# Kernel tuning notes

Hardware: AMD Instinct MI355X
Metric: run time of the kernel (lower is better)

Reference implementation:

```python
import jax, jax.numpy as jnp
import numpy as np

B, L, H, N = 8, 8192, 128, 32  # batch, seq_len, d_model, d_state//2 (complex)


def setup_inputs() -> dict:
    key = jax.random.key(0)
    ks = jax.random.split(key, 13)
    x = jax.random.normal(ks[0], (B, L, 2), dtype=jnp.float32)
    enc_w = jax.random.normal(ks[1], (2, H), dtype=jnp.float32) * (1.0 / np.sqrt(2.0))
    enc_b = jax.random.normal(ks[2], (H,), dtype=jnp.float32) * 0.01
    # S4D init: dt log-uniform in [1e-3, 1e-1], A = -0.5 + i*pi*n (S4D-Lin)
    u01 = jax.random.uniform(ks[3], (H,), dtype=jnp.float32)
    log_dt = u01 * (np.log(0.1) - np.log(0.001)) + np.log(0.001)
    log_A_real = jnp.full((H, N), np.log(0.5), dtype=jnp.float32)
    A_imag = jnp.broadcast_to(np.pi * jnp.arange(N, dtype=jnp.float32), (H, N)).copy()
    C_re = jax.random.normal(ks[4], (H, N), dtype=jnp.float32) * (0.5 ** 0.5)
    C_im = jax.random.normal(ks[5], (H, N), dtype=jnp.float32) * (0.5 ** 0.5)
    D = jax.random.normal(ks[6], (H,), dtype=jnp.float32)
    out_w = jax.random.normal(ks[7], (2 * H, H), dtype=jnp.float32) * (1.0 / np.sqrt(H))
    out_b = jax.random.normal(ks[8], (2 * H,), dtype=jnp.float32) * 0.01
    dec_w = jax.random.normal(ks[9], (H, 1), dtype=jnp.float32) * (1.0 / np.sqrt(H))
    dec_b = jax.random.normal(ks[10], (1,), dtype=jnp.float32) * 0.01
    return {"x": x, "enc_w": enc_w, "enc_b": enc_b, "log_dt": log_dt,
            "log_A_real": log_A_real, "A_imag": A_imag, "C_re": C_re,
            "C_im": C_im, "D": D, "out_w": out_w, "out_b": out_b,
            "dec_w": dec_w, "dec_b": dec_b}


def reference(x, enc_w, enc_b, log_dt, log_A_real, A_imag, C_re, C_im, D,
              out_w, out_b, dec_w, dec_b):
    # Encoder (B,L,2) -> (B,L,H), then transpose to channels-first (B,H,L)
    u = jnp.einsum('blc,ch->blh', x, enc_w) + enc_b
    u = jnp.swapaxes(u, -1, -2)  # (B,H,L)
    Lx = u.shape[-1]

    # --- S4D kernel (zero-order-hold discretization, diagonal A) ---
    dt = jnp.exp(log_dt)                      # (H,)
    A = -jnp.exp(log_A_real) + 1j * A_imag    # (H,N) complex
    C = C_re + 1j * C_im                      # (H,N)
    dtA = dt[:, None] * A                     # (H,N)
    K_coef = C * (jnp.exp(dtA) - 1.0) / A     # (H,N)
    # Vandermonde: exp(dtA * l), l = 0..L-1  -> (H,N,L)
    vand = jnp.exp(dtA[:, :, None] * jnp.arange(Lx, dtype=jnp.float32))
    K = 2.0 * jnp.einsum('hn,hnl->hl', K_coef, vand).real  # (H,L)

    # --- causal convolution via FFT (length 2L avoids circular wrap) ---
    n = 2 * Lx
    y = jnp.fft.irfft(jnp.fft.rfft(u, n) * jnp.fft.rfft(K, n), n)[..., :Lx]
    y = y + D[:, None] * u                    # skip connection

    # GELU -> pointwise GLU output projection (Conv1d(H, 2H, 1) + GLU)
    y = jax.nn.gelu(y)
    z = jnp.einsum('bhl,gh->bgl', y, out_w) + out_b[None, :, None]  # (B,2H,L)
    a, g = jnp.split(z, 2, axis=1)
    y = a * jax.nn.sigmoid(g)                 # (B,H,L)

    # Mean-pool over sequence, decode to scalar: (B,1)
    pooled = jnp.mean(y, axis=-1)             # (B,H)
    return pooled @ dec_w + dec_b
```

## Files before the change

kernel.cpp:

```cpp
#include <hip/hip_runtime.h>
#include <math.h>

#define B_ 8
#define L_ 8192
#define H_ 128
#define N_ 32
#define C_ 128
#define T_ 64


typedef _Float16 half8 __attribute__((ext_vector_type(8)));
typedef __attribute__((ext_vector_type(4))) float f32x4;

__device__ __forceinline__ float gelu_tanh(float y) {
    float t = 0.7978845608028654f * fmaf(0.044715f, y * y * y, y);
    float e = __expf(2.f * t);
    float th = 1.f - __fdividef(2.f, e + 1.f);
    return 0.5f * y * (1.f + th);
}
__device__ __forceinline__ unsigned short f2h(float f) {
    _Float16 h = (_Float16)f;
    return *(unsigned short*)&h;
}
__device__ __forceinline__ float h2f(unsigned short u) {
    return (float)(*(const _Float16*)&u);
}

__global__ __launch_bounds__(256) void k_s4d(
    const float* __restrict__ x, const float* __restrict__ enc_w,
    const float* __restrict__ enc_b, const float* __restrict__ log_dt,
    const float* __restrict__ log_A_real, const float* __restrict__ A_imag,
    const float* __restrict__ C_re, const float* __restrict__ C_im,
    const float* __restrict__ Dp, const float* __restrict__ out_w,
    unsigned short* __restrict__ Wh, unsigned short* __restrict__ gy)
{
    const int bh = blockIdx.x;
    const int b = bh >> 7, h = bh & (H_ - 1);
    const int tid = threadIdx.x;
    const int lane = tid & 63, wq = tid >> 6;
    const int mrow = lane & 15, quad = lane >> 4;

    __shared__ unsigned short Ut[C_][72];
    __shared__ __align__(16) char scratch[18432];
    __shared__ float2 wTpow[7][N_];
    __shared__ float2 coefs[N_];
    __shared__ float2 ArAi[N_];
    __shared__ float  Kd[64];
    unsigned short* E16 = (unsigned short*)scratch;
    float2*         Sx  = (float2*)scratch;
    unsigned short* St  = (unsigned short*)scratch;

    const float dt = expf(log_dt[h]);

    if (tid < N_) {
        int n = tid;
        float Ar = -expf(log_A_real[h * N_ + n]);
        float Ai = A_imag[h * N_ + n];
        ArAi[n] = make_float2(Ar, Ai);
        float ar = dt * Ar, ai = dt * Ai;
        float er = expf(ar);
        float wr = er * cosf(ai), wi = er * sinf(ai);
        float inv = 1.f / (Ar * Ar + Ai * Ai);
        float numr = wr - 1.f, numi = wi;
        float qr = (numr * Ar + numi * Ai) * inv;
        float qi = (numi * Ar - numr * Ai) * inv;
        coefs[n] = make_float2(C_re[h * N_ + n] * qr - C_im[h * N_ + n] * qi,
                               C_re[h * N_ + n] * qi + C_im[h * N_ + n] * qr);
        float arT = dt * Ar * (float)T_, aiT = dt * Ai * (float)T_;
        float erT = expf(arT);
        float pr = erT * cosf(aiT), pi = erT * sinf(aiT);
#pragma unroll
        for (int k = 0; k < 7; ++k) {
            wTpow[k][n] = make_float2(pr, pi);
            float nr = pr * pr - pi * pi;
            pi = 2.f * pr * pi; pr = nr;
        }
    }

    if (b == 0) {
        int g = 2 * h + (tid >> 7), j = tid & 127;
        Wh[g * 128 + j] = f2h(out_w[g * 128 + j]);
    }

    const float ew0 = enc_w[h], ew1 = enc_w[H_ + h], eb = enc_b[h];
    {
        int c = tid >> 1, j0 = (tid & 1) * 32;
        const float4* xp = (const float4*)((const float2*)x + (size_t)b * L_
                                           + c * 64 + j0);
#pragma unroll
        for (int i = 0; i < 16; ++i) {
            float4 xv = xp[i];
            float u0 = fmaf(xv.x, ew0, fmaf(xv.y, ew1, eb));
            float u1 = fmaf(xv.z, ew0, fmaf(xv.w, ew1, eb));
            unsigned int pk = (unsigned)f2h(u0) | ((unsigned)f2h(u1) << 16);
            *(unsigned int*)&Ut[c][j0 + 2 * i] = pk;
        }
    }
    __syncthreads();

    {
        int t = tid >> 2, q = tid & 3;
        float s = 0.f;
        float ft = (float)t;
#pragma unroll
        for (int k = 0; k < 8; ++k) {
            int n = q * 8 + k;
            float2 cf = coefs[n]; float2 aa = ArAi[n];
            float er = __expf(dt * aa.x * ft);
            float sn, cs; __sincosf(dt * aa.y * ft, &sn, &cs);
            s = fmaf(cf.x, er * cs, s);
            s = fmaf(-cf.y, er * sn, s);
        }
        ((float*)&Ut[t][64])[q] = s;
    }

    {
        f32x4 acc[8];
#pragma unroll
        for (int nt = 0; nt < 8; ++nt) acc[nt] = (f32x4){0.f, 0.f, 0.f, 0.f};
        const int m = wq * 16 + mrow;
        const float2 aa = ArAi[m & 31];
        const float dAr = dt * aa.x, dAi = dt * aa.y;
        const bool isIm = (m >= 32);
#pragma unroll
        for (int ks = 0; ks < 2; ++ks) {
            int k0 = ks * 32 + quad * 8;
            half8 af;
#pragma unroll
            for (int i = 0; i < 8; ++i) {
                float d = (float)(63 - (k0 + i));
                float er = __expf(dAr * d);
                float sn, cs; __sincosf(dAi * d, &sn, &cs);
                af[i] = (_Float16)(isIm ? er * sn : er * cs);
            }
#pragma unroll
            for (int nt = 0; nt < 8; ++nt) {
                half8 bf = *(const half8*)&Ut[nt * 16 + mrow][k0];
                acc[nt] = __builtin_amdgcn_mfma_f32_16x16x32_f16(
                    af, bf, acc[nt], 0, 0, 0);
            }
        }
#pragma unroll
        for (int nt = 0; nt < 8; ++nt) {
            int cc = nt * 16 + mrow;
#pragma unroll
            for (int r = 0; r < 4; ++r)
                E16[(wq * 16 + quad * 4 + r) * 136 + cc] = f2h(acc[nt][r]);
        }
    }
    __syncthreads();

    if (tid < 64) {
        const float* kp = (const float*)&Ut[tid][64];
        Kd[tid] = 2.f * (kp[0] + kp[1] + kp[2] + kp[3]);
    }

    float zr[16], zi[16];
    const int cHalf = wq & 1, nHalf = wq >> 1;
    const int n0 = nHalf * 16;
    const int c = cHalf * 64 + lane;
#pragma unroll
    for (int j = 0; j < 16; ++j) {
        zr[j] = h2f(E16[(n0 + j) * 136 + c]);
        zi[j] = h2f(E16[(32 + n0 + j) * 136 + c]);
    }
    __syncthreads();
#pragma unroll
    for (int k = 0; k < 6; ++k) {
        int s = 1 << k;
        float mask = (lane >= s) ? 1.f : 0.f;
#pragma unroll
        for (int j = 0; j < 16; ++j) {
            float2 q = wTpow[k][n0 + j];
            float vr = __shfl_up(zr[j], s, 64);
            float vi = __shfl_up(zi[j], s, 64);
            float adr = fmaf(q.x, vr, -(q.y * vi));
            float adi = fmaf(q.x, vi, q.y * vr);
            zr[j] = fmaf(mask, adr, zr[j]);
            zi[j] = fmaf(mask, adi, zi[j]);
        }
    }
    if (cHalf == 0) {
#pragma unroll
        for (int j = 0; j < 16; ++j)
            Sx[(n0 + j) * 64 + lane] = make_float2(zr[j], zi[j]);
    }
    __syncthreads();
    if (cHalf == 1) {
#pragma unroll
        for (int j = 0; j < 16; ++j) {
            float2 q = wTpow[6][n0 + j];
            float2 v = Sx[(n0 + j) * 64 + lane];
            zr[j] = fmaf(q.x, v.x, fmaf(-q.y, v.y, zr[j]));
            zi[j] = fmaf(q.x, v.y, fmaf(q.y, v.x, zi[j]));
        }
    }
    {
        bool l0 = (lane == 0);
#pragma unroll
        for (int j = 0; j < 16; ++j) {
            float2 bv = Sx[(n0 + j) * 64 + 63];
            float br = (cHalf == 1) ? bv.x : 0.f;
            float bi = (cHalf == 1) ? bv.y : 0.f;
            float tr = __shfl_up(zr[j], 1, 64);
            float ti = __shfl_up(zi[j], 1, 64);
            zr[j] = l0 ? br : tr;
            zi[j] = l0 ? bi : ti;
        }
    }
    __syncthreads();
    {
#pragma unroll
        for (int j2 = 0; j2 < 8; ++j2) {
            unsigned int p0 = (unsigned)f2h(zr[2 * j2]) |
                              ((unsigned)f2h(zr[2 * j2 + 1]) << 16);
            unsigned int p1 = (unsigned)f2h(zi[2 * j2]) |
                              ((unsigned)f2h(zi[2 * j2 + 1]) << 16);
            *(unsigned int*)&St[c * 72 + n0 + 2 * j2] = p0;
            *(unsigned int*)&St[c * 72 + 32 + n0 + 2 * j2] = p1;
        }
    }
    __syncthreads();

    {
        f32x4 acc[8];
#pragma unroll
        for (int nt = 0; nt < 8; ++nt) acc[nt] = (f32x4){0.f, 0.f, 0.f, 0.f};
        const int t = wq * 16 + mrow;
#pragma unroll
        for (int ks = 0; ks < 2; ++ks) {
            int k0 = ks * 32 + quad * 8;
            half8 af;
#pragma unroll
            for (int i = 0; i < 8; ++i) {
                int j = k0 + i;
                af[i] = (_Float16)((t >= j) ? Kd[t - j] : 0.f);
            }
#pragma unroll
            for (int nt = 0; nt < 8; ++nt) {
                half8 bf = *(const half8*)&Ut[nt * 16 + mrow][k0];
                acc[nt] = __builtin_amdgcn_mfma_f32_16x16x32_f16(
                    af, bf, acc[nt], 0, 0, 0);
            }
        }
        half8 afP0, afP1;
        {
            float tp1 = (float)(t + 1);
#pragma unroll
            for (int i = 0; i < 8; ++i) {
                int n = quad * 8 + i;
                float2 cf = coefs[n]; float2 aa = ArAi[n];
                float er = __expf(dt * aa.x * tp1);
                float sn, cs; __sincosf(dt * aa.y * tp1, &sn, &cs);
                float wr = er * cs, wi = er * sn;
                afP0[i] = (_Float16)( 2.f * (cf.x * wr - cf.y * wi));
                afP1[i] = (_Float16)(-2.f * (cf.x * wi + cf.y * wr));
            }
        }
#pragma unroll
        for (int ks = 0; ks < 2; ++ks) {
            int k0 = ks * 32 + quad * 8;
            half8 af = ks ? afP1 : afP0;
#pragma unroll
            for (int nt = 0; nt < 8; ++nt) {
                half8 bf = *(const half8*)&St[(nt * 16 + mrow) * 72 + k0];
                acc[nt] = __builtin_amdgcn_mfma_f32_16x16x32_f16(
                    af, bf, acc[nt], 0, 0, 0);
            }
        }
        const float Dh = Dp[h];
        unsigned short* gyb = gy + (size_t)bh * L_;
#pragma unroll
        for (int nt = 0; nt < 8; ++nt) {
            int cc = nt * 16 + mrow;
#pragma unroll
            for (int r = 0; r < 4; ++r) {
                int tt = wq * 16 + quad * 4 + r;
                float u = h2f(Ut[cc][tt]);
                float y = fmaf(Dh, u, acc[nt][r]);
                gyb[tt * 128 + cc] = f2h(gelu_tanh(y));
            }
        }
    }
}

#define BPAD 136
__global__ __launch_bounds__(256) void k_mix(
    const unsigned short* __restrict__ Wh, const unsigned short* __restrict__ gy,
    const float* __restrict__ out_b, const float* __restrict__ dec_w,
    float* __restrict__ part)
{
    __shared__ unsigned short Bt[64 * BPAD];
    __shared__ float red[4];

    const int blk = blockIdx.x;
    const int b = blk >> 7;
    const int t = (blk >> 1) & 63, ch = blk & 1;
    const int tid = threadIdx.x;
    const int wq = tid >> 6, lane = tid & 63;

    const unsigned short* gsrc = gy + (size_t)(b * H_) * L_ + t * 128 + ch * 64;
#pragma unroll
    for (int it = 0; it < 4; ++it) {
        int idx = it * 256 + tid;
        int h = idx >> 3, v0 = (idx & 7) * 8;
        uint4 q = *(const uint4*)(gsrc + (size_t)h * L_ + v0);
        Bt[(v0 + 0) * BPAD + h] = (unsigned short)(q.x & 0xFFFF);
        Bt[(v0 + 1) * BPAD + h] = (unsigned short)(q.x >> 16);
        Bt[(v0 + 2) * BPAD + h] = (unsigned short)(q.y & 0xFFFF);
        Bt[(v0 + 3) * BPAD + h] = (unsigned short)(q.y >> 16);
        Bt[(v0 + 4) * BPAD + h] = (unsigned short)(q.z & 0xFFFF);
        Bt[(v0 + 5) * BPAD + h] = (unsigned short)(q.z >> 16);
        Bt[(v0 + 6) * BPAD + h] = (unsigned short)(q.w & 0xFFFF);
        Bt[(v0 + 7) * BPAD + h] = (unsigned short)(q.w >> 16);
    }
    __syncthreads();

    const int ga = wq * 32;
    const int gg = 128 + wq * 32;
    const int mrow = lane & 15;
    const int quad = lane >> 4;
    f32x4 accA[2][4], accG[2][4];
#pragma unroll
    for (int mt = 0; mt < 2; ++mt)
#pragma unroll
        for (int nt = 0; nt < 4; ++nt) {
            accA[mt][nt] = (f32x4){0.f, 0.f, 0.f, 0.f};
            accG[mt][nt] = (f32x4){0.f, 0.f, 0.f, 0.f};
        }

#pragma unroll
    for (int k = 0; k < 4; ++k) {
        const int h0 = k * 32 + quad * 8;
        half8 bfr[4];
#pragma unroll
        for (int nt = 0; nt < 4; ++nt) {
            int v = nt * 16 + mrow;
            bfr[nt] = *(const half8*)(Bt + v * BPAD + h0);
        }
#pragma unroll
        for (int mt = 0; mt < 2; ++mt) {
            half8 ah = *(const half8*)(Wh + (ga + mt * 16 + mrow) * 128 + h0);
            half8 ag = *(const half8*)(Wh + (gg + mt * 16 + mrow) * 128 + h0);
#pragma unroll
            for (int nt = 0; nt < 4; ++nt) {
                accA[mt][nt] = __builtin_amdgcn_mfma_f32_16x16x32_f16(
                    ah, bfr[nt], accA[mt][nt], 0, 0, 0);
                accG[mt][nt] = __builtin_amdgcn_mfma_f32_16x16x32_f16(
                    ag, bfr[nt], accG[mt][nt], 0, 0, 0);
            }
        }
    }

    float s = 0.f;
#pragma unroll
    for (int mt = 0; mt < 2; ++mt) {
        float4 obA = *(const float4*)(out_b + ga + mt * 16 + quad * 4);
        float4 obG = *(const float4*)(out_b + gg + mt * 16 + quad * 4);
        float4 dv  = *(const float4*)(dec_w + ga + mt * 16 + quad * 4);
#pragma unroll
        for (int nt = 0; nt < 4; ++nt) {
#pragma unroll
            for (int r = 0; r < 4; ++r) {
                float a  = accA[mt][nt][r] + ((const float*)&obA)[r];
                float zg = accG[mt][nt][r] + ((const float*)&obG)[r];
                float sig = __fdividef(1.f, 1.f + __expf(-zg));
                s = fmaf(((const float*)&dv)[r], a * sig, s);
            }
        }
    }
#pragma unroll
    for (int off = 32; off; off >>= 1) s += __shfl_down(s, off, 64);
    if (lane == 0) red[wq] = s;
    __syncthreads();
    if (tid == 0) part[blk] = red[0] + red[1] + red[2] + red[3];
}

__global__ __launch_bounds__(512) void k_final(
    const float* __restrict__ part, const float* __restrict__ dec_b,
    float* __restrict__ out)
{
    int tid = threadIdx.x;
    int b = tid >> 6, lane = tid & 63;
    float s = part[b * 128 + lane] + part[b * 128 + 64 + lane];
#pragma unroll
    for (int off = 32; off; off >>= 1) s += __shfl_down(s, off, 64);
    if (lane == 0) out[b] = fmaf(s, 1.0f / (float)L_, dec_b[0]);
}

extern "C" void kernel_launch(void* const* d_in, const int* in_sizes, int n_in,
                              void* d_out, int out_size, void* d_ws, size_t ws_size,
                              hipStream_t stream)
{
    const float* x         = (const float*)d_in[0];
    const float* enc_w     = (const float*)d_in[1];
    const float* enc_b     = (const float*)d_in[2];
    const float* log_dt    = (const float*)d_in[3];
    const float* log_A_real= (const float*)d_in[4];
    const float* A_imag    = (const float*)d_in[5];
    const float* C_re      = (const float*)d_in[6];
    const float* C_im      = (const float*)d_in[7];
    const float* Dp        = (const float*)d_in[8];
    const float* out_w     = (const float*)d_in[9];
    const float* out_b     = (const float*)d_in[10];
    const float* dec_w     = (const float*)d_in[11];
    const float* dec_b     = (const float*)d_in[12];
    float* out = (float*)d_out;

    char* ws = (char*)d_ws;
    unsigned short* Wh = (unsigned short*)(ws);
    unsigned short* gy = (unsigned short*)(ws + 3211264);
    float* part        = (float*)(ws + 19988480);

    k_s4d<<<B_ * H_, 256, 0, stream>>>(x, enc_w, enc_b, log_dt, log_A_real,
                                       A_imag, C_re, C_im, Dp, out_w, Wh, gy);
    k_mix<<<B_ * 128, 256, 0, stream>>>(Wh, gy, out_b, dec_w, part);
    k_final<<<1, 512, 0, stream>>>(part, dec_b, out);
}
```

Before: 132.5 us.

## Fuse final reduction into mix kernel, fold D into kernel, vectorize LDS traffic

The separate final-reduction kernel is removed: the last k_mix block, found through an atomic counter, sums the partials and writes the output, which saves one launch. The D skip term is folded into the first convolution tap, so the per-element u reload disappears. The E16 layout is transposed so that stores and loads use packed 64-bit and 128-bit LDS accesses, and the z-state stores become uint4 writes. The k_mix B-tile drops its padding in favour of an XOR swizzle. These changes add atomic ordering concerns and swizzle complexity.

```diff
diff --git a/kernel.cpp b/kernel.cpp
--- a/kernel.cpp
+++ b/kernel.cpp
@@ -25,6 +25,9 @@
 __device__ __forceinline__ float h2f(unsigned short u) {
     return (float)(*(const _Float16*)&u);
 }
+__device__ __forceinline__ unsigned int pk2(float a, float b) {
+    return (unsigned)f2h(a) | ((unsigned)f2h(b) << 16);
+}
 
 __global__ __launch_bounds__(256) void k_s4d(
     const float* __restrict__ x, const float* __restrict__ enc_w,
@@ -32,7 +35,8 @@
     const float* __restrict__ log_A_real, const float* __restrict__ A_imag,
     const float* __restrict__ C_re, const float* __restrict__ C_im,
     const float* __restrict__ Dp, const float* __restrict__ out_w,
-    unsigned short* __restrict__ Wh, unsigned short* __restrict__ gy)
+    unsigned short* __restrict__ Wh, unsigned short* __restrict__ gy,
+    unsigned int* __restrict__ cnt)
 {
     const int bh = blockIdx.x;
     const int b = bh >> 7, h = bh & (H_ - 1);
@@ -50,7 +54,10 @@
     float2*         Sx  = (float2*)scratch;
     unsigned short* St  = (unsigned short*)scratch;
 
+    if (bh == 0 && tid == 0) *cnt = 0;
+
     const float dt = expf(log_dt[h]);
+    const float Dh = Dp[h];
 
     if (tid < N_) {
         int n = tid;
@@ -92,8 +99,7 @@
             float4 xv = xp[i];
             float u0 = fmaf(xv.x, ew0, fmaf(xv.y, ew1, eb));
             float u1 = fmaf(xv.z, ew0, fmaf(xv.w, ew1, eb));
-            unsigned int pk = (unsigned)f2h(u0) | ((unsigned)f2h(u1) << 16);
-            *(unsigned int*)&Ut[c][j0 + 2 * i] = pk;
+            *(unsigned int*)&Ut[c][j0 + 2 * i] = pk2(u0, u1);
         }
     }
     __syncthreads();
@@ -140,29 +146,38 @@
                     af, bf, acc[nt], 0, 0, 0);
             }
         }
+        const int m0 = wq * 16 + quad * 4;
 #pragma unroll
         for (int nt = 0; nt < 8; ++nt) {
             int cc = nt * 16 + mrow;
-#pragma unroll
-            for (int r = 0; r < 4; ++r)
-                E16[(wq * 16 + quad * 4 + r) * 136 + cc] = f2h(acc[nt][r]);
+            unsigned long long w =
+                (unsigned long long)pk2(acc[nt][0], acc[nt][1]) |
+                ((unsigned long long)pk2(acc[nt][2], acc[nt][3]) << 32);
+            *(unsigned long long*)&E16[cc * 72 + m0] = w;
         }
     }
     __syncthreads();
 
     if (tid < 64) {
         const float* kp = (const float*)&Ut[tid][64];
-        Kd[tid] = 2.f * (kp[0] + kp[1] + kp[2] + kp[3]);
+        Kd[tid] = 2.f * (kp[0] + kp[1] + kp[2] + kp[3])
+                  + ((tid == 0) ? Dh : 0.f);
     }
 
     float zr[16], zi[16];
     const int cHalf = wq & 1, nHalf = wq >> 1;
     const int n0 = nHalf * 16;
     const int c = cHalf * 64 + lane;
-#pragma unroll
-    for (int j = 0; j < 16; ++j) {
-        zr[j] = h2f(E16[(n0 + j) * 136 + c]);
-        zi[j] = h2f(E16[(32 + n0 + j) * 136 + c]);
+    {
+        half8 ha = *(const half8*)(E16 + c * 72 + n0);
+        half8 hb = *(const half8*)(E16 + c * 72 + n0 + 8);
+        half8 hc = *(const half8*)(E16 + c * 72 + 32 + n0);
+        half8 hd = *(const half8*)(E16 + c * 72 + 32 + n0 + 8);
+#pragma unroll
+        for (int j = 0; j < 8; ++j) {
+            zr[j] = (float)ha[j];  zr[8 + j] = (float)hb[j];
+            zi[j] = (float)hc[j];  zi[8 + j] = (float)hd[j];
+        }
     }
     __syncthreads();
 #pragma unroll
@@ -210,15 +225,19 @@
     }
     __syncthreads();
     {
-#pragma unroll
-        for (int j2 = 0; j2 < 8; ++j2) {
-            unsigned int p0 = (unsigned)f2h(zr[2 * j2]) |
-                              ((unsigned)f2h(zr[2 * j2 + 1]) << 16);
-            unsigned int p1 = (unsigned)f2h(zi[2 * j2]) |
-                              ((unsigned)f2h(zi[2 * j2 + 1]) << 16);
-            *(unsigned int*)&St[c * 72 + n0 + 2 * j2] = p0;
-            *(unsigned int*)&St[c * 72 + 32 + n0 + 2 * j2] = p1;
-        }
+        uint4 w0, w1;
+        w0.x = pk2(zr[0], zr[1]);   w0.y = pk2(zr[2], zr[3]);
+        w0.z = pk2(zr[4], zr[5]);   w0.w = pk2(zr[6], zr[7]);
+        w1.x = pk2(zr[8], zr[9]);   w1.y = pk2(zr[10], zr[11]);
+        w1.z = pk2(zr[12], zr[13]); w1.w = pk2(zr[14], zr[15]);
+        *(uint4*)&St[c * 72 + n0] = w0;
+        *(uint4*)&St[c * 72 + n0 + 8] = w1;
+        w0.x = pk2(zi[0], zi[1]);   w0.y = pk2(zi[2], zi[3]);
+        w0.z = pk2(zi[4], zi[5]);   w0.w = pk2(zi[6], zi[7]);
+        w1.x = pk2(zi[8], zi[9]);   w1.y = pk2(zi[10], zi[11]);
+        w1.z = pk2(zi[12], zi[13]); w1.w = pk2(zi[14], zi[15]);
+        *(uint4*)&St[c * 72 + 32 + n0] = w0;
+        *(uint4*)&St[c * 72 + 32 + n0 + 8] = w1;
     }
     __syncthreads();
 
@@ -268,7 +287,6 @@
                     af, bf, acc[nt], 0, 0, 0);
             }
         }
-        const float Dh = Dp[h];
         unsigned short* gyb = gy + (size_t)bh * L_;
 #pragma unroll
         for (int nt = 0; nt < 8; ++nt) {
@@ -276,22 +294,21 @@
 #pragma unroll
             for (int r = 0; r < 4; ++r) {
                 int tt = wq * 16 + quad * 4 + r;
-                float u = h2f(Ut[cc][tt]);
-                float y = fmaf(Dh, u, acc[nt][r]);
-                gyb[tt * 128 + cc] = f2h(gelu_tanh(y));
-            }
-        }
-    }
-}
-
-#define BPAD 136
+                gyb[tt * 128 + cc] = f2h(gelu_tanh(acc[nt][r]));
+            }
+        }
+    }
+}
+
 __global__ __launch_bounds__(256) void k_mix(
     const unsigned short* __restrict__ Wh, const unsigned short* __restrict__ gy,
     const float* __restrict__ out_b, const float* __restrict__ dec_w,
-    float* __restrict__ part)
+    const float* __restrict__ dec_b, float* __restrict__ part,
+    unsigned int* __restrict__ cnt, float* __restrict__ out)
 {
-    __shared__ unsigned short Bt[64 * BPAD];
+    __shared__ unsigned short Bt[64 * 128];
     __shared__ float red[4];
+    __shared__ int isLast;
 
     const int blk = blockIdx.x;
     const int b = blk >> 7;
@@ -305,14 +322,15 @@
         int idx = it * 256 + tid;
         int h = idx >> 3, v0 = (idx & 7) * 8;
         uint4 q = *(const uint4*)(gsrc + (size_t)h * L_ + v0);
-        Bt[(v0 + 0) * BPAD + h] = (unsigned short)(q.x & 0xFFFF);
-        Bt[(v0 + 1) * BPAD + h] = (unsigned short)(q.x >> 16);
-        Bt[(v0 + 2) * BPAD + h] = (unsigned short)(q.y & 0xFFFF);
-        Bt[(v0 + 3) * BPAD + h] = (unsigned short)(q.y >> 16);
-        Bt[(v0 + 4) * BPAD + h] = (unsigned short)(q.z & 0xFFFF);
-        Bt[(v0 + 5) * BPAD + h] = (unsigned short)(q.z >> 16);
-        Bt[(v0 + 6) * BPAD + h] = (unsigned short)(q.w & 0xFFFF);
-        Bt[(v0 + 7) * BPAD + h] = (unsigned short)(q.w >> 16);
+        const int sw = (((h >> 3) ^ (idx & 7)) << 3) | (h & 7);
+        Bt[(v0 + 0) * 128 + sw] = (unsigned short)(q.x & 0xFFFF);
+        Bt[(v0 + 1) * 128 + sw] = (unsigned short)(q.x >> 16);
+        Bt[(v0 + 2) * 128 + sw] = (unsigned short)(q.y & 0xFFFF);
+        Bt[(v0 + 3) * 128 + sw] = (unsigned short)(q.y >> 16);
+        Bt[(v0 + 4) * 128 + sw] = (unsigned short)(q.z & 0xFFFF);
+        Bt[(v0 + 5) * 128 + sw] = (unsigned short)(q.z >> 16);
+        Bt[(v0 + 6) * 128 + sw] = (unsigned short)(q.w & 0xFFFF);
+        Bt[(v0 + 7) * 128 + sw] = (unsigned short)(q.w >> 16);
     }
     __syncthreads();
 
@@ -336,7 +354,8 @@
 #pragma unroll
         for (int nt = 0; nt < 4; ++nt) {
             int v = nt * 16 + mrow;
-            bfr[nt] = *(const half8*)(Bt + v * BPAD + h0);
+            bfr[nt] = *(const half8*)&Bt[v * 128 +
+                                         (((4 * k + quad) ^ (v >> 3)) << 3)];
         }
 #pragma unroll
         for (int mt = 0; mt < 2; ++mt) {
@@ -373,19 +392,28 @@
     for (int off = 32; off; off >>= 1) s += __shfl_down(s, off, 64);
     if (lane == 0) red[wq] = s;
     __syncthreads();
-    if (tid == 0) part[blk] = red[0] + red[1] + red[2] + red[3];
-}
-
-__global__ __launch_bounds__(512) void k_final(
-    const float* __restrict__ part, const float* __restrict__ dec_b,
-    float* __restrict__ out)
-{
-    int tid = threadIdx.x;
-    int b = tid >> 6, lane = tid & 63;
-    float s = part[b * 128 + lane] + part[b * 128 + 64 + lane];
-#pragma unroll
-    for (int off = 32; off; off >>= 1) s += __shfl_down(s, off, 64);
-    if (lane == 0) out[b] = fmaf(s, 1.0f / (float)L_, dec_b[0]);
+    if (tid == 0) {
+        float total = red[0] + red[1] + red[2] + red[3];
+        __hip_atomic_store(&part[blk], total, __ATOMIC_RELAXED,
+                           __HIP_MEMORY_SCOPE_AGENT);
+        unsigned int old = __hip_atomic_fetch_add(cnt, 1u, __ATOMIC_ACQ_REL,
+                                                  __HIP_MEMORY_SCOPE_AGENT);
+        isLast = (old == (unsigned)(B_ * 128 - 1));
+    }
+    __syncthreads();
+    if (!isLast) return;
+
+    {
+        int b2 = tid >> 5, i = tid & 31;
+        float sum = 0.f;
+#pragma unroll
+        for (int k = 0; k < 4; ++k)
+            sum += __hip_atomic_load(&part[b2 * 128 + i + 32 * k],
+                                     __ATOMIC_RELAXED, __HIP_MEMORY_SCOPE_AGENT);
+#pragma unroll
+        for (int off = 16; off; off >>= 1) sum += __shfl_down(sum, off, 32);
+        if (i == 0) out[b2] = fmaf(sum, 1.0f / (float)L_, dec_b[0]);
+    }
 }
 
 extern "C" void kernel_launch(void* const* d_in, const int* in_sizes, int n_in,
@@ -411,9 +439,11 @@
     unsigned short* Wh = (unsigned short*)(ws);
     unsigned short* gy = (unsigned short*)(ws + 3211264);
     float* part        = (float*)(ws + 19988480);
+    unsigned int* cnt  = (unsigned int*)(ws + 19992576);
 
     k_s4d<<<B_ * H_, 256, 0, stream>>>(x, enc_w, enc_b, log_dt, log_A_real,
-                                       A_imag, C_re, C_im, Dp, out_w, Wh, gy);
-    k_mix<<<B_ * 128, 256, 0, stream>>>(Wh, gy, out_b, dec_w, part);
-    k_final<<<1, 512, 0, stream>>>(part, dec_b, out);
-}
+                                       A_imag, C_re, C_im, Dp, out_w, Wh, gy,
+                                       cnt);
+    k_mix<<<B_ * 128, 256, 0, stream>>>(Wh, gy, out_b, dec_w, dec_b, part,
+                                        cnt, out);
+}
```

After: 144.8 us. 9.3% more time.
